# Performance work log

Measured on AMD Instinct MI355X. Metric: run time of the kernel, lower is better.

## Reference

```python
import jax, jax.numpy as jnp
import numpy as np

SQRT_DK = jnp.sqrt(jnp.float32(128.0))
BN_EPS = 1e-5


def setup_inputs() -> dict:
    key = jax.random.key(0)
    ks = jax.random.split(key, 12)
    B, C, F, Fp, K, O, DK = 4, 64, 20000, 10000, 16, 128, 128
    fea = jax.random.normal(ks[0], (B, C, F), dtype=jnp.float32)
    ring_n = jax.random.randint(ks[1], (B, Fp, K), 0, F, dtype=jnp.int64)
    pool_idx = jnp.sort(jax.random.randint(ks[2], (Fp,), 0, F, dtype=jnp.int64))
    pos_embed = jnp.zeros((1, 1, 1), dtype=jnp.float32)
    s = 1.0 / np.sqrt(C)
    Wk = jax.random.uniform(ks[3], (DK, C), jnp.float32, -s, s)
    bk = jax.random.uniform(ks[4], (DK,), jnp.float32, -s, s)
    Wq = jax.random.uniform(ks[5], (DK, C), jnp.float32, -s, s)
    bq = jax.random.uniform(ks[6], (DK,), jnp.float32, -s, s)
    Wc = jax.random.uniform(ks[7], (O, C), jnp.float32, -s, s)
    bc = jax.random.uniform(ks[8], (O,), jnp.float32, -s, s)
    gamma = jnp.ones((O,), jnp.float32)
    beta = jnp.zeros((O,), jnp.float32)
    return {"fea": fea, "ring_n": ring_n, "pool_idx": pool_idx, "pos_embed": pos_embed,
            "Wk": Wk, "bk": bk, "Wq": Wq, "bq": bq, "Wc": Wc, "bc": bc,
            "gamma": gamma, "beta": beta}


def _gather_neighbors(fea, ring_n):
    # fea: [B,C,F], ring_n: [B,Fp,K] -> [B,C,Fp,K]
    return jax.vmap(lambda f, r: f[:, r])(fea, ring_n)


def reference(fea, ring_n, pool_idx, pos_embed, Wk, bk, Wq, bq, Wc, bc, gamma, beta):
    # neighbor gather along face dim
    neighbor_fea = _gather_neighbors(fea, ring_n)            # [B,C,Fp,K]
    self_fea = fea[:, :, pool_idx][..., None]                # [B,C,Fp,1]
    cat = jnp.concatenate([self_fea, neighbor_fea], axis=3)  # [B,C,Fp,K+1]
    # per-face key (self only) and per-neighbor query (Linear4D over channel dim)
    keyv = jnp.einsum('bcfk,oc->bofk', self_fea, Wk) + bk[None, :, None, None]  # [B,128,Fp,1]
    query = jnp.einsum('bcfk,oc->bofk', cat, Wq) + bq[None, :, None, None]       # [B,128,Fp,K+1]
    att = jnp.sum(keyv * query, axis=1, keepdims=True) / SQRT_DK                 # [B,1,Fp,K+1]
    att = jax.nn.softmax(att, axis=3)
    agg = jnp.sum(cat * att, axis=3)                                             # [B,C,Fp]
    # concat_mlp: 1x1 conv + BatchNorm1d (training-mode batch stats) + ReLU
    y = jnp.einsum('bcf,oc->bof', agg, Wc) + bc[None, :, None]                   # [B,O,Fp]
    mean = jnp.mean(y, axis=(0, 2), keepdims=True)
    var = jnp.var(y, axis=(0, 2), keepdims=True)
    y = (y - mean) * jax.lax.rsqrt(var + BN_EPS)
    y = y * gamma[None, :, None] + beta[None, :, None]
    return jax.nn.relu(y)
```

## Files before the change

kernel.cpp:

```cpp
#include <hip/hip_runtime.h>

#define F_ALL 20000
#define FP    10000
#define BB    4
#define CC    64
#define KK    16
#define OO    128
#define NFACE (BB*FP)
#define NELEM (BB*OO*FP)
#define NGRAMB 125

#define WS_AGG  0
#define WS_MT   (NFACE*64)
#define WS_V0   (WS_MT + 4096)
#define WS_G    (WS_V0 + 64)
#define WS_SUMA (WS_G + 4096)
#define WS_SC   (WS_SUMA + 64)
#define WS_SH   (WS_SC + 128)

template<int CTRL>
__device__ __forceinline__ float dpp_add(float x) {
    return x + __int_as_float(__builtin_amdgcn_update_dpp(0, __float_as_int(x), CTRL, 0xF, 0xF, true));
}
__device__ __forceinline__ float sum16(float x) {
    x = dpp_add<0x121>(x);
    x = dpp_add<0x122>(x);
    x = dpp_add<0x124>(x);
    x = dpp_add<0x128>(x);
    return x;
}

__global__ __launch_bounds__(256) void k_transpose(const float* __restrict__ fea,
                                                   float* __restrict__ feaT) {
    __shared__ float tile[64][65];
    int bb = blockIdx.x / 313;
    int tb = blockIdx.x % 313;
    int fbase = tb * 64;
    int tid = threadIdx.x;
    int x  = tid & 63;
    int y0 = tid >> 6;
    int f = fbase + x;
    if (f < F_ALL) {
#pragma unroll
        for (int i = 0; i < 16; i++) {
            int c = y0 + i * 4;
            tile[c][x] = fea[((long)bb * CC + c) * F_ALL + f];
        }
    }
    __syncthreads();
#pragma unroll
    for (int i = 0; i < 16; i++) {
        int fr = y0 + i * 4;
        int ff = fbase + fr;
        if (ff < F_ALL)
            feaT[((long)bb * F_ALL + ff) * 64 + x] = tile[x][fr];
    }
}

__global__ __launch_bounds__(256) void k_precompute(const float* __restrict__ Wk,
                                                    const float* __restrict__ bk,
                                                    const float* __restrict__ Wq,
                                                    float* __restrict__ ws) {
    int idx = blockIdx.x * 256 + threadIdx.x;
    int j = idx >> 6, i = idx & 63;
    float acc = 0.f;
#pragma unroll 8
    for (int o = 0; o < 128; o++) acc += Wq[o * 64 + i] * Wk[o * 64 + j];
    ws[WS_MT + idx] = acc;
    if (blockIdx.x == 0 && threadIdx.x < 64) {
        int t = threadIdx.x;
        float a = 0.f;
        for (int o = 0; o < 128; o++) a += Wq[o * 64 + t] * bk[o];
        ws[WS_V0 + t] = a;
    }
}

__global__ __launch_bounds__(256) void k_qvec(const float* __restrict__ feaT,
                                              const int* __restrict__ pool,
                                              float* __restrict__ ws) {
    __shared__ float At[4096];
    __shared__ float Sf[64 * 65];
    int tid = threadIdx.x;
    int fbase = blockIdx.x * 64;

    for (int i = tid; i < 4096; i += 256) At[i] = ws[WS_MT + i];
    {
        int r = tid >> 2;
        int face = fbase + r;
        int b = face / FP;
        int fp = face - b * FP;
        int p = pool[fp];
        const float* src = feaT + ((long)(b * F_ALL + p)) * 64;
        int off = (tid & 3) * 4;
#pragma unroll
        for (int it = 0; it < 4; it++, off += 16) {
            float4 v = *(const float4*)(src + off);
            Sf[r * 65 + off + 0] = v.x;
            Sf[r * 65 + off + 1] = v.y;
            Sf[r * 65 + off + 2] = v.z;
            Sf[r * 65 + off + 3] = v.w;
        }
    }
    __syncthreads();

    int ti = tid & 15, tj = tid >> 4;
    int f0 = ti * 4, o0 = tj * 4;
    float4 v0 = *(const float4*)&ws[WS_V0 + o0];
    float acc[4][4];
#pragma unroll
    for (int a = 0; a < 4; a++) {
        acc[a][0] = v0.x; acc[a][1] = v0.y; acc[a][2] = v0.z; acc[a][3] = v0.w;
    }
    for (int j = 0; j < 64; j++) {
        float4 wv = *(const float4*)&At[j * 64 + o0];
#pragma unroll
        for (int a = 0; a < 4; a++) {
            float av = Sf[(f0 + a) * 65 + j];
            acc[a][0] += av * wv.x;
            acc[a][1] += av * wv.y;
            acc[a][2] += av * wv.z;
            acc[a][3] += av * wv.w;
        }
    }
#pragma unroll
    for (int a = 0; a < 4; a++)
        *(float4*)&ws[WS_AGG + ((long)(fbase + f0 + a)) * 64 + o0] =
            make_float4(acc[a][0], acc[a][1], acc[a][2], acc[a][3]);
}

__global__ __launch_bounds__(256) void k_attn(const float* __restrict__ feaT,
                                              const int* __restrict__ ring,
                                              const int* __restrict__ pool,
                                              float* __restrict__ ws) {
    int tid = threadIdx.x;
    int lane = tid & 63;
    int il = lane & 15;
    int c4 = il * 4;
    int face = blockIdx.x * 16 + (tid >> 4);
    int b  = face / FP;
    int fp = face - b * FP;
    const float* fb = feaT + ((long)b * F_ALL) * 64 + c4;
    const float scale = 0.08838834764831845f;

    int p = pool[fp];
    float4 sf = *(const float4*)(fb + (long)p * 64);
    float4 u  = *(const float4*)&ws[WS_AGG + (long)face * 64 + c4];

    int rv = ring[face * KK + il];
    float4 nv[KK];
#pragma unroll
    for (int k = 0; k < KK; k++) {
        int rk = __shfl(rv, (lane & 48) | k, 64);
        nv[k] = *(const float4*)(fb + (long)rk * 64);
    }

    float l[KK + 1];
    l[0] = sum16(u.x * sf.x + u.y * sf.y + u.z * sf.z + u.w * sf.w) * scale;
#pragma unroll
    for (int k = 0; k < KK; k++)
        l[k + 1] = sum16(u.x * nv[k].x + u.y * nv[k].y + u.z * nv[k].z + u.w * nv[k].w) * scale;

    float m = l[0];
#pragma unroll
    for (int k = 1; k <= KK; k++) m = fmaxf(m, l[k]);
    float den = 0.f;
#pragma unroll
    for (int k = 0; k <= KK; k++) { l[k] = __expf(l[k] - m); den += l[k]; }
    float inv = 1.0f / den;

    float4 a;
    a.x = l[0] * sf.x; a.y = l[0] * sf.y; a.z = l[0] * sf.z; a.w = l[0] * sf.w;
#pragma unroll
    for (int k = 0; k < KK; k++) {
        a.x += l[k + 1] * nv[k].x;
        a.y += l[k + 1] * nv[k].y;
        a.z += l[k + 1] * nv[k].z;
        a.w += l[k + 1] * nv[k].w;
    }
    a.x *= inv; a.y *= inv; a.z *= inv; a.w *= inv;
    *(float4*)&ws[WS_AGG + (long)face * 64 + c4] = a;
}

__global__ __launch_bounds__(256) void k_gram(const float* __restrict__ agg,
                                              float* __restrict__ gp,
                                              float* __restrict__ sap) {
    __shared__ float lbuf[4096];
    int tid = threadIdx.x;
    int ti = tid & 15, tj = tid >> 4;
    float acc[4][4];
#pragma unroll
    for (int a = 0; a < 4; a++)
#pragma unroll
        for (int b = 0; b < 4; b++) acc[a][b] = 0.f;
    float gacc[4] = {0.f, 0.f, 0.f, 0.f};

    for (int c = 0; c < 5; c++) {
        int fbase = blockIdx.x * 320 + c * 64;
        const float4* src = (const float4*)(agg + (long)fbase * 64);
        float4* dst = (float4*)lbuf;
        for (int i = tid; i < 1024; i += 256) dst[i] = src[i];
        __syncthreads();
#pragma unroll 4
        for (int f = 0; f < 64; f++) {
            float4 av = *(const float4*)&lbuf[f * 64 + ti * 4];
            float4 bv = *(const float4*)&lbuf[f * 64 + tj * 4];
            float avv[4] = {av.x, av.y, av.z, av.w};
            float bvv[4] = {bv.x, bv.y, bv.z, bv.w};
#pragma unroll
            for (int a = 0; a < 4; a++) {
#pragma unroll
                for (int b = 0; b < 4; b++) acc[a][b] += avv[a] * bvv[b];
                gacc[a] += avv[a];
            }
        }
        __syncthreads();
    }
#pragma unroll
    for (int a = 0; a < 4; a++)
        *(float4*)&gp[(long)blockIdx.x * 4096 + (ti * 4 + a) * 64 + tj * 4] =
            make_float4(acc[a][0], acc[a][1], acc[a][2], acc[a][3]);
    if (tj == 0)
        *(float4*)&sap[blockIdx.x * 64 + ti * 4] =
            make_float4(gacc[0], gacc[1], gacc[2], gacc[3]);
}

__global__ __launch_bounds__(256) void k_gsum(const float* __restrict__ gp,
                                              const float* __restrict__ sap,
                                              float* __restrict__ ws) {
    if (blockIdx.x < 16) {
        int e = blockIdx.x * 256 + threadIdx.x;
        float s = 0.f;
#pragma unroll 5
        for (int p = 0; p < NGRAMB; p++) s += gp[(long)p * 4096 + e];
        ws[WS_G + e] = s;
    } else if (threadIdx.x < 64) {
        float s = 0.f;
#pragma unroll 5
        for (int p = 0; p < NGRAMB; p++) s += sap[p * 64 + threadIdx.x];
        ws[WS_SUMA + threadIdx.x] = s;
    }
}

__global__ __launch_bounds__(256) void k_stats(const float* __restrict__ Wc,
                                               const float* __restrict__ bc,
                                               const float* __restrict__ gamma,
                                               const float* __restrict__ beta,
                                               float* __restrict__ ws) {
    __shared__ float Gs[4096];
    __shared__ float gs[64];
    __shared__ float qs[256];
    int tid = threadIdx.x;
    for (int i = tid; i < 4096; i += 256) Gs[i] = ws[WS_G + i];
    if (tid < 64) gs[tid] = ws[WS_SUMA + tid];
    __syncthreads();

    int o = tid & 127, h = tid >> 7;
    float w[64];
#pragma unroll
    for (int q = 0; q < 16; q++) {
        float4 t = *(const float4*)&Wc[o * 64 + q * 4];
        w[q * 4 + 0] = t.x; w[q * 4 + 1] = t.y; w[q * 4 + 2] = t.z; w[q * 4 + 3] = t.w;
    }
    float qp = 0.f;
    for (int i = h * 32; i < h * 32 + 32; i++) {
        float t = 0.f;
#pragma unroll
        for (int j = 0; j < 64; j++) t += Gs[i * 64 + j] * w[j];
        qp += Wc[o * 64 + i] * t;
    }
    qs[tid] = qp;
    __syncthreads();
    if (h == 0) {
        const float invN = 1.0f / (float)NFACE;
        float qform = qs[o] + qs[o + 128];
        float md = 0.f;
#pragma unroll
        for (int j = 0; j < 64; j++) md += gs[j] * w[j];
        float bco = bc[o];
        float mean = md * invN + bco;
        float ey2  = (qform + 2.f * bco * md) * invN + bco * bco;
        float var  = ey2 - mean * mean;
        float sc   = gamma[o] * rsqrtf(var + 1e-5f);
        ws[WS_SC + o] = sc;
        ws[WS_SH + o] = beta[o] + (bco - mean) * sc;
    }
}

__global__ __launch_bounds__(256) void k_out(const float* __restrict__ agg,
                                             const float* __restrict__ Wc,
                                             const float* __restrict__ ws,
                                             float* __restrict__ out) {
    __shared__ __align__(16) float WcT[64 * 132];
    __shared__ __align__(16) float AgT[64 * 68];
    int tid = threadIdx.x;
    int fbase = blockIdx.x * 64;
    for (int i = tid; i < 128 * 64; i += 256) {
        int o = i >> 6, j = i & 63;
        WcT[j * 132 + o] = Wc[i];
    }
    for (int i = tid; i < 64 * 64; i += 256) {
        int f = i >> 6, j = i & 63;
        AgT[j * 68 + f] = agg[((long)(fbase + f)) * 64 + j];
    }
    __syncthreads();

    int tx = tid & 15, ty = tid >> 4;
    float acc[8][4];
#pragma unroll
    for (int a = 0; a < 8; a++)
#pragma unroll
        for (int b = 0; b < 4; b++) acc[a][b] = 0.f;

    for (int j = 0; j < 64; j++) {
        float4 w0 = *(const float4*)&WcT[j * 132 + ty * 8];
        float4 w1 = *(const float4*)&WcT[j * 132 + ty * 8 + 4];
        float4 a0 = *(const float4*)&AgT[j * 68 + tx * 4];
        float wv[8] = {w0.x, w0.y, w0.z, w0.w, w1.x, w1.y, w1.z, w1.w};
        float av[4] = {a0.x, a0.y, a0.z, a0.w};
#pragma unroll
        for (int oi = 0; oi < 8; oi++)
#pragma unroll
            for (int fi = 0; fi < 4; fi++) acc[oi][fi] += wv[oi] * av[fi];
    }

    int fg0 = fbase + tx * 4;
    int b   = fg0 / FP;
    int fp0 = fg0 - b * FP;
#pragma unroll
    for (int oi = 0; oi < 8; oi++) {
        int o = ty * 8 + oi;
        float sc = ws[WS_SC + o];
        float sh = ws[WS_SH + o];
        float4 v;
        v.x = fmaxf(acc[oi][0] * sc + sh, 0.f);
        v.y = fmaxf(acc[oi][1] * sc + sh, 0.f);
        v.z = fmaxf(acc[oi][2] * sc + sh, 0.f);
        v.w = fmaxf(acc[oi][3] * sc + sh, 0.f);
        *(float4*)&out[((long)(b * OO + o)) * FP + fp0] = v;
    }
}

extern "C" void kernel_launch(void* const* d_in, const int* in_sizes, int n_in,
                              void* d_out, int out_size, void* d_ws, size_t ws_size,
                              hipStream_t stream) {
    const float* fea  = (const float*)d_in[0];
    const int*   ring = (const int*)d_in[1];
    const int*   pool = (const int*)d_in[2];
    const float* Wk = (const float*)d_in[4];
    const float* bk = (const float*)d_in[5];
    const float* Wq = (const float*)d_in[6];
    const float* Wc = (const float*)d_in[8];
    const float* bc = (const float*)d_in[9];
    const float* gamma = (const float*)d_in[10];
    const float* beta  = (const float*)d_in[11];

    float* out  = (float*)d_out;
    float* ws   = (float*)d_ws;
    float* feaT = out;
    float* agg  = ws + WS_AGG;
    float* gp   = out;
    float* sap  = out + NGRAMB * 4096;

    k_transpose <<<dim3(BB * 313), 256, 0, stream>>>(fea, feaT);
    k_precompute<<<16,   256, 0, stream>>>(Wk, bk, Wq, ws);
    k_qvec      <<<625,  256, 0, stream>>>(feaT, pool, ws);
    k_attn      <<<2500, 256, 0, stream>>>(feaT, ring, pool, ws);
    k_gram      <<<NGRAMB, 256, 0, stream>>>(agg, gp, sap);
    k_gsum      <<<17,   256, 0, stream>>>(gp, sap, ws);
    k_stats     <<<1,    256, 0, stream>>>(Wc, bc, gamma, beta, ws);
    k_out       <<<625,  256, 0, stream>>>(agg, Wc, ws, out);
}
```

Before: 195.5 us.

## Fuse qvec, attention and Gram partials into one kernel; merge transpose with precompute

Merges the transpose and weight precompute into one launch, and fuses the query-vector GEMM, neighbor attention, and per-block Gram/sum partials into a single 64-face-per-block kernel. Intermediates (u vectors, self features, aggregated features) stay in LDS instead of round-tripping through global memory. Launch count drops from eight to five. In exchange, the Gram partial count grows from 125 to 625, so the reduction kernel is reworked to split each sum across four thread groups. The transposed features and partials now live in the workspace rather than the output buffer, and the larger LDS footprint per block may reduce occupancy in the attention phase.

```diff
diff --git a/kernel.cpp b/kernel.cpp
--- a/kernel.cpp
+++ b/kernel.cpp
@@ -3,15 +3,16 @@
 #define F_ALL 20000
 #define FP    10000
 #define BB    4
-#define CC    64
 #define KK    16
 #define OO    128
-#define NFACE (BB*FP)
-#define NELEM (BB*OO*FP)
-#define NGRAMB 125
-
-#define WS_AGG  0
-#define WS_MT   (NFACE*64)
+#define NFACE 40000
+#define NBLK  625
+
+#define WS_FEAT 0
+#define WS_AGG  (BB*F_ALL*64)
+#define WS_GP   (WS_AGG + NFACE*64)
+#define WS_SAP  (WS_GP + NBLK*4096)
+#define WS_MT   (WS_SAP + NBLK*64)
 #define WS_V0   (WS_MT + 4096)
 #define WS_G    (WS_V0 + 64)
 #define WS_SUMA (WS_G + 4096)
@@ -30,66 +31,69 @@
     return x;
 }
 
-__global__ __launch_bounds__(256) void k_transpose(const float* __restrict__ fea,
-                                                   float* __restrict__ feaT) {
+__global__ __launch_bounds__(256) void k_pre(const float* __restrict__ fea,
+                                             const float* __restrict__ Wk,
+                                             const float* __restrict__ bk,
+                                             const float* __restrict__ Wq,
+                                             float* __restrict__ ws) {
     __shared__ float tile[64][65];
-    int bb = blockIdx.x / 313;
-    int tb = blockIdx.x % 313;
-    int fbase = tb * 64;
     int tid = threadIdx.x;
-    int x  = tid & 63;
-    int y0 = tid >> 6;
-    int f = fbase + x;
-    if (f < F_ALL) {
+    if (blockIdx.x < 1252) {
+        int bb = blockIdx.x / 313;
+        int tb = blockIdx.x % 313;
+        int fbase = tb * 64;
+        int x  = tid & 63;
+        int y0 = tid >> 6;
+        int f = fbase + x;
+        float* feaT = ws + WS_FEAT;
+        if (f < F_ALL) {
+#pragma unroll
+            for (int i = 0; i < 16; i++) {
+                int c = y0 + i * 4;
+                tile[c][x] = fea[((long)bb * 64 + c) * F_ALL + f];
+            }
+        }
+        __syncthreads();
 #pragma unroll
         for (int i = 0; i < 16; i++) {
-            int c = y0 + i * 4;
-            tile[c][x] = fea[((long)bb * CC + c) * F_ALL + f];
-        }
-    }
-    __syncthreads();
-#pragma unroll
-    for (int i = 0; i < 16; i++) {
-        int fr = y0 + i * 4;
-        int ff = fbase + fr;
-        if (ff < F_ALL)
-            feaT[((long)bb * F_ALL + ff) * 64 + x] = tile[x][fr];
-    }
-}
-
-__global__ __launch_bounds__(256) void k_precompute(const float* __restrict__ Wk,
-                                                    const float* __restrict__ bk,
-                                                    const float* __restrict__ Wq,
-                                                    float* __restrict__ ws) {
-    int idx = blockIdx.x * 256 + threadIdx.x;
-    int j = idx >> 6, i = idx & 63;
-    float acc = 0.f;
+            int fr = y0 + i * 4;
+            int ff = fbase + fr;
+            if (ff < F_ALL)
+                feaT[((long)bb * F_ALL + ff) * 64 + x] = tile[x][fr];
+        }
+    } else {
+        int idx = (blockIdx.x - 1252) * 256 + tid;
+        int j = idx >> 6, i = idx & 63;
+        float acc = 0.f;
 #pragma unroll 8
-    for (int o = 0; o < 128; o++) acc += Wq[o * 64 + i] * Wk[o * 64 + j];
-    ws[WS_MT + idx] = acc;
-    if (blockIdx.x == 0 && threadIdx.x < 64) {
-        int t = threadIdx.x;
-        float a = 0.f;
-        for (int o = 0; o < 128; o++) a += Wq[o * 64 + t] * bk[o];
-        ws[WS_V0 + t] = a;
-    }
-}
-
-__global__ __launch_bounds__(256) void k_qvec(const float* __restrict__ feaT,
+        for (int o = 0; o < 128; o++) acc += Wq[o * 64 + i] * Wk[o * 64 + j];
+        ws[WS_MT + idx] = acc;
+        if (blockIdx.x == 1252 && tid < 64) {
+            float a = 0.f;
+            for (int o = 0; o < 128; o++) a += Wq[o * 64 + tid] * bk[o];
+            ws[WS_V0 + tid] = a;
+        }
+    }
+}
+
+__global__ __launch_bounds__(256) void k_attn(const int* __restrict__ ring,
                                               const int* __restrict__ pool,
                                               float* __restrict__ ws) {
-    __shared__ float At[4096];
-    __shared__ float Sf[64 * 65];
+    __shared__ __align__(16) float lds[12608];
+    float* At = lds;
+    float* Sf = lds + 4096;
+    float* U  = lds + 8256;
     int tid = threadIdx.x;
     int fbase = blockIdx.x * 64;
+    const float* feaT = ws + WS_FEAT;
+    const float scale = 0.08838834764831845f;
 
     for (int i = tid; i < 4096; i += 256) At[i] = ws[WS_MT + i];
     {
         int r = tid >> 2;
         int face = fbase + r;
         int b = face / FP;
-        int fp = face - b * FP;
-        int p = pool[fp];
+        int p = pool[face - b * FP];
         const float* src = feaT + ((long)(b * F_ALL + p)) * 64;
         int off = (tid & 3) * 4;
 #pragma unroll
@@ -104,140 +108,132 @@
     __syncthreads();
 
     int ti = tid & 15, tj = tid >> 4;
-    int f0 = ti * 4, o0 = tj * 4;
-    float4 v0 = *(const float4*)&ws[WS_V0 + o0];
-    float acc[4][4];
-#pragma unroll
-    for (int a = 0; a < 4; a++) {
-        acc[a][0] = v0.x; acc[a][1] = v0.y; acc[a][2] = v0.z; acc[a][3] = v0.w;
-    }
-    for (int j = 0; j < 64; j++) {
-        float4 wv = *(const float4*)&At[j * 64 + o0];
+    {
+        int f0 = ti * 4, o0 = tj * 4;
+        float4 v0 = *(const float4*)&ws[WS_V0 + o0];
+        float acc[4][4];
 #pragma unroll
         for (int a = 0; a < 4; a++) {
-            float av = Sf[(f0 + a) * 65 + j];
-            acc[a][0] += av * wv.x;
-            acc[a][1] += av * wv.y;
-            acc[a][2] += av * wv.z;
-            acc[a][3] += av * wv.w;
-        }
-    }
-#pragma unroll
-    for (int a = 0; a < 4; a++)
-        *(float4*)&ws[WS_AGG + ((long)(fbase + f0 + a)) * 64 + o0] =
-            make_float4(acc[a][0], acc[a][1], acc[a][2], acc[a][3]);
-}
-
-__global__ __launch_bounds__(256) void k_attn(const float* __restrict__ feaT,
-                                              const int* __restrict__ ring,
-                                              const int* __restrict__ pool,
-                                              float* __restrict__ ws) {
-    int tid = threadIdx.x;
+            acc[a][0] = v0.x; acc[a][1] = v0.y; acc[a][2] = v0.z; acc[a][3] = v0.w;
+        }
+        for (int j = 0; j < 64; j++) {
+            float4 wv = *(const float4*)&At[j * 64 + o0];
+#pragma unroll
+            for (int a = 0; a < 4; a++) {
+                float av = Sf[(f0 + a) * 65 + j];
+                acc[a][0] += av * wv.x;
+                acc[a][1] += av * wv.y;
+                acc[a][2] += av * wv.z;
+                acc[a][3] += av * wv.w;
+            }
+        }
+#pragma unroll
+        for (int a = 0; a < 4; a++)
+            *(float4*)&U[(f0 + a) * 68 + o0] =
+                make_float4(acc[a][0], acc[a][1], acc[a][2], acc[a][3]);
+    }
+    __syncthreads();
+
+    float* Ag = At;
     int lane = tid & 63;
-    int il = lane & 15;
-    int c4 = il * 4;
-    int face = blockIdx.x * 16 + (tid >> 4);
-    int b  = face / FP;
-    int fp = face - b * FP;
-    const float* fb = feaT + ((long)b * F_ALL) * 64 + c4;
-    const float scale = 0.08838834764831845f;
-
-    int p = pool[fp];
-    float4 sf = *(const float4*)(fb + (long)p * 64);
-    float4 u  = *(const float4*)&ws[WS_AGG + (long)face * 64 + c4];
-
-    int rv = ring[face * KK + il];
-    float4 nv[KK];
-#pragma unroll
-    for (int k = 0; k < KK; k++) {
-        int rk = __shfl(rv, (lane & 48) | k, 64);
-        nv[k] = *(const float4*)(fb + (long)rk * 64);
-    }
-
-    float l[KK + 1];
-    l[0] = sum16(u.x * sf.x + u.y * sf.y + u.z * sf.z + u.w * sf.w) * scale;
-#pragma unroll
-    for (int k = 0; k < KK; k++)
-        l[k + 1] = sum16(u.x * nv[k].x + u.y * nv[k].y + u.z * nv[k].z + u.w * nv[k].w) * scale;
-
-    float m = l[0];
-#pragma unroll
-    for (int k = 1; k <= KK; k++) m = fmaxf(m, l[k]);
-    float den = 0.f;
-#pragma unroll
-    for (int k = 0; k <= KK; k++) { l[k] = __expf(l[k] - m); den += l[k]; }
-    float inv = 1.0f / den;
-
-    float4 a;
-    a.x = l[0] * sf.x; a.y = l[0] * sf.y; a.z = l[0] * sf.z; a.w = l[0] * sf.w;
-#pragma unroll
-    for (int k = 0; k < KK; k++) {
-        a.x += l[k + 1] * nv[k].x;
-        a.y += l[k + 1] * nv[k].y;
-        a.z += l[k + 1] * nv[k].z;
-        a.w += l[k + 1] * nv[k].w;
-    }
-    a.x *= inv; a.y *= inv; a.z *= inv; a.w *= inv;
-    *(float4*)&ws[WS_AGG + (long)face * 64 + c4] = a;
-}
-
-__global__ __launch_bounds__(256) void k_gram(const float* __restrict__ agg,
-                                              float* __restrict__ gp,
-                                              float* __restrict__ sap) {
-    __shared__ float lbuf[4096];
-    int tid = threadIdx.x;
-    int ti = tid & 15, tj = tid >> 4;
+    int il = lane & 15, c4 = il * 4;
+    for (int it = 0; it < 4; it++) {
+        int fl = (tid >> 4) + it * 16;
+        int face = fbase + fl;
+        int b = face / FP;
+        const float* fb = feaT + ((long)b * F_ALL) * 64 + c4;
+
+        float4 sf = make_float4(Sf[fl * 65 + c4], Sf[fl * 65 + c4 + 1],
+                                Sf[fl * 65 + c4 + 2], Sf[fl * 65 + c4 + 3]);
+        float4 u = *(const float4*)&U[fl * 68 + c4];
+
+        int rv = ring[face * KK + il];
+        float4 nv[KK];
+#pragma unroll
+        for (int k = 0; k < KK; k++) {
+            int rk = __shfl(rv, (lane & 48) | k, 64);
+            nv[k] = *(const float4*)(fb + (long)rk * 64);
+        }
+
+        float l[KK + 1];
+        l[0] = sum16(u.x * sf.x + u.y * sf.y + u.z * sf.z + u.w * sf.w) * scale;
+#pragma unroll
+        for (int k = 0; k < KK; k++)
+            l[k + 1] = sum16(u.x * nv[k].x + u.y * nv[k].y + u.z * nv[k].z + u.w * nv[k].w) * scale;
+
+        float m = l[0];
+#pragma unroll
+        for (int k = 1; k <= KK; k++) m = fmaxf(m, l[k]);
+        float den = 0.f;
+#pragma unroll
+        for (int k = 0; k <= KK; k++) { l[k] = __expf(l[k] - m); den += l[k]; }
+        float inv = 1.0f / den;
+
+        float4 a;
+        a.x = l[0] * sf.x; a.y = l[0] * sf.y; a.z = l[0] * sf.z; a.w = l[0] * sf.w;
+#pragma unroll
+        for (int k = 0; k < KK; k++) {
+            a.x += l[k + 1] * nv[k].x;
+            a.y += l[k + 1] * nv[k].y;
+            a.z += l[k + 1] * nv[k].z;
+            a.w += l[k + 1] * nv[k].w;
+        }
+        a.x *= inv; a.y *= inv; a.z *= inv; a.w *= inv;
+        *(float4*)&Ag[fl * 64 + c4] = a;
+        *(float4*)&ws[WS_AGG + (long)face * 64 + c4] = a;
+    }
+    __syncthreads();
+
     float acc[4][4];
 #pragma unroll
     for (int a = 0; a < 4; a++)
 #pragma unroll
         for (int b = 0; b < 4; b++) acc[a][b] = 0.f;
     float gacc[4] = {0.f, 0.f, 0.f, 0.f};
-
-    for (int c = 0; c < 5; c++) {
-        int fbase = blockIdx.x * 320 + c * 64;
-        const float4* src = (const float4*)(agg + (long)fbase * 64);
-        float4* dst = (float4*)lbuf;
-        for (int i = tid; i < 1024; i += 256) dst[i] = src[i];
-        __syncthreads();
 #pragma unroll 4
-        for (int f = 0; f < 64; f++) {
-            float4 av = *(const float4*)&lbuf[f * 64 + ti * 4];
-            float4 bv = *(const float4*)&lbuf[f * 64 + tj * 4];
-            float avv[4] = {av.x, av.y, av.z, av.w};
-            float bvv[4] = {bv.x, bv.y, bv.z, bv.w};
-#pragma unroll
-            for (int a = 0; a < 4; a++) {
-#pragma unroll
-                for (int b = 0; b < 4; b++) acc[a][b] += avv[a] * bvv[b];
-                gacc[a] += avv[a];
-            }
-        }
-        __syncthreads();
-    }
+    for (int f = 0; f < 64; f++) {
+        float4 av = *(const float4*)&Ag[f * 64 + ti * 4];
+        float4 bv = *(const float4*)&Ag[f * 64 + tj * 4];
+        float avv[4] = {av.x, av.y, av.z, av.w};
+        float bvv[4] = {bv.x, bv.y, bv.z, bv.w};
+#pragma unroll
+        for (int a = 0; a < 4; a++) {
+#pragma unroll
+            for (int b = 0; b < 4; b++) acc[a][b] += avv[a] * bvv[b];
+            gacc[a] += avv[a];
+        }
+    }
+    float* gp = ws + WS_GP;
 #pragma unroll
     for (int a = 0; a < 4; a++)
         *(float4*)&gp[(long)blockIdx.x * 4096 + (ti * 4 + a) * 64 + tj * 4] =
             make_float4(acc[a][0], acc[a][1], acc[a][2], acc[a][3]);
     if (tj == 0)
-        *(float4*)&sap[blockIdx.x * 64 + ti * 4] =
+        *(float4*)&ws[WS_SAP + blockIdx.x * 64 + ti * 4] =
             make_float4(gacc[0], gacc[1], gacc[2], gacc[3]);
 }
 
-__global__ __launch_bounds__(256) void k_gsum(const float* __restrict__ gp,
-                                              const float* __restrict__ sap,
-                                              float* __restrict__ ws) {
-    if (blockIdx.x < 16) {
-        int e = blockIdx.x * 256 + threadIdx.x;
+__global__ __launch_bounds__(256) void k_gsum(float* __restrict__ ws) {
+    __shared__ float red[256];
+    const float* gp  = ws + WS_GP;
+    const float* sap = ws + WS_SAP;
+    int t = threadIdx.x;
+    int e = t & 63, pc = t >> 6;
+    int p0 = pc * 157;
+    int p1 = p0 + 157; if (p1 > NBLK) p1 = NBLK;
+    if (blockIdx.x < 64) {
+        int eg = blockIdx.x * 64 + e;
         float s = 0.f;
-#pragma unroll 5
-        for (int p = 0; p < NGRAMB; p++) s += gp[(long)p * 4096 + e];
-        ws[WS_G + e] = s;
-    } else if (threadIdx.x < 64) {
+        for (int p = p0; p < p1; p++) s += gp[(long)p * 4096 + eg];
+        red[t] = s;
+        __syncthreads();
+        if (pc == 0) ws[WS_G + eg] = red[e] + red[e + 64] + red[e + 128] + red[e + 192];
+    } else {
         float s = 0.f;
-#pragma unroll 5
-        for (int p = 0; p < NGRAMB; p++) s += sap[p * 64 + threadIdx.x];
-        ws[WS_SUMA + threadIdx.x] = s;
+        for (int p = p0; p < p1; p++) s += sap[p * 64 + e];
+        red[t] = s;
+        __syncthreads();
+        if (pc == 0) ws[WS_SUMA + e] = red[e] + red[e + 64] + red[e + 128] + red[e + 192];
     }
 }
 
@@ -286,12 +282,12 @@
     }
 }
 
-__global__ __launch_bounds__(256) void k_out(const float* __restrict__ agg,
-                                             const float* __restrict__ Wc,
+__global__ __launch_bounds__(256) void k_out(const float* __restrict__ Wc,
                                              const float* __restrict__ ws,
                                              float* __restrict__ out) {
     __shared__ __align__(16) float WcT[64 * 132];
     __shared__ __align__(16) float AgT[64 * 68];
+    const float* agg = ws + WS_AGG;
     int tid = threadIdx.x;
     int fbase = blockIdx.x * 64;
     for (int i = tid; i < 128 * 64; i += 256) {
@@ -354,19 +350,12 @@
     const float* gamma = (const float*)d_in[10];
     const float* beta  = (const float*)d_in[11];
 
-    float* out  = (float*)d_out;
-    float* ws   = (float*)d_ws;
-    float* feaT = out;
-    float* agg  = ws + WS_AGG;
-    float* gp   = out;
-    float* sap  = out + NGRAMB * 4096;
-
-    k_transpose <<<dim3(BB * 313), 256, 0, stream>>>(fea, feaT);
-    k_precompute<<<16,   256, 0, stream>>>(Wk, bk, Wq, ws);
-    k_qvec      <<<625,  256, 0, stream>>>(feaT, pool, ws);
-    k_attn      <<<2500, 256, 0, stream>>>(feaT, ring, pool, ws);
-    k_gram      <<<NGRAMB, 256, 0, stream>>>(agg, gp, sap);
-    k_gsum      <<<17,   256, 0, stream>>>(gp, sap, ws);
-    k_stats     <<<1,    256, 0, stream>>>(Wc, bc, gamma, beta, ws);
-    k_out       <<<625,  256, 0, stream>>>(agg, Wc, ws, out);
-}
+    float* out = (float*)d_out;
+    float* ws  = (float*)d_ws;
+
+    k_pre  <<<1268, 256, 0, stream>>>(fea, Wk, bk, Wq, ws);
+    k_attn <<<NBLK, 256, 0, stream>>>(ring, pool, ws);
+    k_gsum <<<65,   256, 0, stream>>>(ws);
+    k_stats<<<1,    256, 0, stream>>>(Wc, bc, gamma, beta, ws);
+    k_out  <<<NBLK, 256, 0, stream>>>(Wc, ws, out);
+}
```

Result: slower. 215.1 us (+10.0%).
